# Kernel tuning notes

Hardware: AMD Instinct MI355X
Metric: run time of the kernel (lower is better)

Reference implementation:

```python
import jax, jax.numpy as jnp
import numpy as np

EPS = 1e-12
NEG_INF = -1e30

def _slog(x):
    return jnp.log(jnp.clip(x, EPS))

def setup_inputs() -> dict:
    M, Z = 24, 1024
    key = jax.random.key(0)
    ks = jax.random.split(key, 20)
    u = lambda k, sh, s=1.0: jax.random.uniform(k, sh, dtype=jnp.float32) * s
    demin = u(ks[0], (M, M), 0.2)
    demax = demin + u(ks[1], (M, M), 1.0)
    Kn = (jax.random.uniform(ks[2], (M, M)) > 0.5).astype(jnp.float32)
    # a couple of sectors with no substitution choices (rows stay all-ones in S)
    Kn = Kn.at[0].set(0.0).at[5].set(0.0)
    housing_mask = jnp.zeros((M,), dtype=bool).at[jnp.array([M - 2, M - 1])].set(True)
    genflux_mask = (jax.random.uniform(ks[3], (M,)) > 0.2)
    return {
        'h': jnp.zeros((M, Z), jnp.float32),
        'price': u(ks[4], (M, Z)),
        't_nij': u(ks[5], (M, Z, Z)),
        'demin': demin,
        'demax': demax,
        'delta': u(ks[6], (M, M), 0.2),
        'omega': u(ks[7], (M, M)),
        'sigma': u(ks[8], (M,), 0.5),
        'Kn': Kn,
        'attractor': u(ks[9], (M, Z)) + 0.1,
        'beta': u(ks[10], (M,), 0.5),
        'lamda': u(ks[11], (M,)),
        'A_ni': u(ks[12], (M, Z)) + 0.1,
        'exog_demand': u(ks[13], (M, Z)),
        'exog_prod': u(ks[14], (M, Z)),
        'X_0': u(ks[15], (M, Z)) + 0.1,
        'X_target': u(ks[16], (M, Z)),
        'housing_mask': housing_mask,
        'genflux_mask': genflux_mask,
    }

def reference(h, price, t_nij, demin, demax, delta, omega, sigma, Kn,
              attractor, beta, lamda, A_ni, exog_demand, exog_prod,
              X_0, X_target, housing_mask, genflux_mask):
    M, Z = price.shape
    ph = price + h                                            # [n,i] prices + shadow prices
    # LocationProbability: U_nij = lamda_n*ph[n,j] + t_nij; Pr = softmax_j for genflux non-housing, else eye
    U_nij = lamda[:, None, None] * ph[:, None, :] + t_nij     # [n,i,j]
    loc_logits = _slog(A_ni)[:, None, :] - beta[:, None, None] * U_nij
    Pr_soft = jax.nn.softmax(loc_logits, axis=-1)
    loc_mask = genflux_mask & (~housing_mask)                 # sectors with location choice
    eye = jnp.eye(Z, dtype=price.dtype)
    Pr = jnp.where(loc_mask[:, None, None], Pr_soft, eye[None, :, :])  # [n,i,j]
    # composite (expected) disutility per sector/zone
    U_ni = jnp.einsum('nij,nij->ni', Pr, U_nij)               # [n,i]
    # DemandFunction: a[m,n,i] = demin + (demax-demin)*exp(-delta*U_ni)
    a_mni = demin[:, :, None] + (demax - demin)[:, :, None] * jnp.exp(-delta[:, :, None] * U_ni[None])
    # SubstitutionProbability: masked softmax over substitutes n (axis=1), S=1 where no choice
    U_tilde = omega[:, :, None] * a_mni * U_ni[None]          # [m,n,i]
    cmask = (Kn > 0)[:, :, None]                              # [m,n,1]
    sub_logits = jnp.where(cmask, _slog(attractor)[None] - sigma[:, None, None] * U_tilde, NEG_INF)
    S_mni = jnp.where(cmask, jax.nn.softmax(sub_logits, axis=1), 1.0)
    # TotalDemand: D[n,i] = exog_demand + sum_m a*S*(X_0+exog_prod)
    X_total = X_0 + exog_prod
    D_ni = exog_demand + jnp.einsum('mni,mni,mi->ni', a_mni, S_mni, X_total)
    # induced production: X_pred[n,j] = sum_i D[n,i] * Pr[n,i,j]
    X_pred = jnp.einsum('ni,nij->nj', D_ni, Pr)
    return jnp.mean((X_pred - X_target) ** 2)
```

## Files before the change

kernel.cpp:

```cpp
#include <hip/hip_runtime.h>
#include <hip/hip_bf16.h>
#include <math.h>

#define MDIM 24
#define ZDIM 1024
#define NEG_INF_F -1e30f
#define EPS_F 1e-12f

enum {
  OFF_U    = 0,
  OFF_RMAX = 24576,
  OFF_SEXP = 49152,
  OFF_W    = 73728,
  OFF_XP   = 98304
};

__device__ __forceinline__ bool masks_are_bytes(const void* hm, const void* gm) {
  const unsigned int* hw = (const unsigned int*)hm;
  const unsigned int* gw = (const unsigned int*)gm;
  bool b = false;
  #pragma unroll
  for (int k = 0; k < 6; k++) {
    unsigned int a = hw[k], c = gw[k];
    if (a != 0u && a != 1u && a != 0x3F800000u) b = true;
    if (c != 0u && c != 1u && c != 0x3F800000u) b = true;
  }
  return b;
}
__device__ __forceinline__ bool loc_flag(const void* hm, const void* gm, int n) {
  bool bytes = masks_are_bytes(hm, gm);
  bool hv = bytes ? (((const unsigned char*)hm)[n] != 0)
                  : (((const unsigned int*)hm)[n] != 0u);
  bool gv = bytes ? (((const unsigned char*)gm)[n] != 0)
                  : (((const unsigned int*)gm)[n] != 0u);
  return gv && !hv;
}

__global__ __launch_bounds__(256) void k1_rows(
    const float* __restrict__ t, const float* __restrict__ price,
    const float* __restrict__ h, const float* __restrict__ A_ni,
    const float* __restrict__ beta, const float* __restrict__ lamda,
    const void* __restrict__ housing, const void* __restrict__ genflux,
    float* __restrict__ ws) {
  const int n  = blockIdx.x >> 6;
  const int i0 = (blockIdx.x & 63) * 16;
  const float bn = beta[n], ln = lamda[n];
  if (!loc_flag(housing, genflux, n)) {
    if (threadIdx.x < 16) {
      const int row = n * ZDIM + i0 + threadIdx.x;
      ws[OFF_U + row] = ln * (price[row] + h[row])
                        + t[(size_t)row * ZDIM + (i0 + threadIdx.x)];
    }
    return;
  }
  __shared__ float pc_s[ZDIM];
  __shared__ float cc_s[ZDIM];
  for (int j = threadIdx.x; j < ZDIM; j += 256) {
    const float pc = ln * (price[n * ZDIM + j] + h[n * ZDIM + j]);
    const float sa = logf(fmaxf(A_ni[n * ZDIM + j], EPS_F));
    pc_s[j] = pc;
    cc_s[j] = sa - bn * pc;
  }
  __syncthreads();
  const int wave = threadIdx.x >> 6, lane = threadIdx.x & 63;
  const float4* pc4 = (const float4*)pc_s;
  const float4* cc4 = (const float4*)cc_s;
  const int r0 = n * ZDIM + i0 + wave * 4;

  float4 tv[4][4];
  #pragma unroll
  for (int r = 0; r < 4; r++) {
    const float4* tp = (const float4*)(t + (size_t)(r0 + r) * ZDIM);
    tv[r][0] = tp[lane];
    tv[r][1] = tp[lane + 64];
    tv[r][2] = tp[lane + 128];
    tv[r][3] = tp[lane + 192];
  }

  #pragma unroll
  for (int r = 0; r < 4; r++) {
    float lg[16], uv[16];
    float mx = -INFINITY;
    #pragma unroll
    for (int k = 0; k < 4; k++) {
      const int f = lane + 64 * k;
      const float4 tt = tv[r][k];
      const float4 pv = pc4[f];
      const float4 cv = cc4[f];
      uv[4*k+0] = pv.x + tt.x;  lg[4*k+0] = cv.x - bn * tt.x;
      uv[4*k+1] = pv.y + tt.y;  lg[4*k+1] = cv.y - bn * tt.y;
      uv[4*k+2] = pv.z + tt.z;  lg[4*k+2] = cv.z - bn * tt.z;
      uv[4*k+3] = pv.w + tt.w;  lg[4*k+3] = cv.w - bn * tt.w;
      mx = fmaxf(mx, fmaxf(fmaxf(lg[4*k], lg[4*k+1]), fmaxf(lg[4*k+2], lg[4*k+3])));
    }
    #pragma unroll
    for (int off = 32; off >= 1; off >>= 1)
      mx = fmaxf(mx, __shfl_xor(mx, off));
    float se = 0.f, su = 0.f;
    #pragma unroll
    for (int k = 0; k < 16; k++) {
      const float e = __expf(lg[k] - mx);
      se += e;
      su = fmaf(e, uv[k], su);
    }
    #pragma unroll
    for (int off = 32; off >= 1; off >>= 1) {
      se += __shfl_xor(se, off);
      su += __shfl_xor(su, off);
    }
    if (lane == 0) {
      const int row = r0 + r;
      ws[OFF_U + row]    = su / se;
      ws[OFF_RMAX + row] = mx;
      ws[OFF_SEXP + row] = se;
    }
  }
}

__global__ __launch_bounds__(256) void k2_demand(
    const float* __restrict__ demin, const float* __restrict__ demax,
    const float* __restrict__ delta, const float* __restrict__ omega,
    const float* __restrict__ sigma, const float* __restrict__ Kn,
    const float* __restrict__ attractor, const float* __restrict__ exogd,
    const float* __restrict__ X0, const float* __restrict__ exogp,
    const void* __restrict__ housing, const void* __restrict__ genflux,
    float* __restrict__ ws) {
  const int wave = threadIdx.x >> 6;
  const int lane = threadIdx.x & 63;
  const int half = lane >> 5;
  const int n    = lane & 31;
  const int i    = blockIdx.x * 8 + wave * 2 + half;
  const bool nv  = (n < MDIM);
  float Uv = 0.f, asl = NEG_INF_F;
  if (nv) {
    Uv  = ws[OFF_U + n * ZDIM + i];
    asl = logf(fmaxf(attractor[n * ZDIM + i], EPS_F));
  }
  float acc = 0.f;
  for (int m = 0; m < MDIM; m++) {
    const float Xt  = X0[m * ZDIM + i] + exogp[m * ZDIM + i];
    const float sig = sigma[m];
    float dm = 0.f, dd = 0.f, dl = 0.f, om = 0.f, kn = 0.f;
    if (nv) {
      dm = demin[m * MDIM + n];
      dd = demax[m * MDIM + n] - dm;
      dl = delta[m * MDIM + n];
      om = omega[m * MDIM + n];
      kn = Kn[m * MDIM + n];
    }
    const float a = dm + dd * __expf(-dl * Uv);
    const bool valid = nv && (kn > 0.f);
    const float l = valid ? asl - sig * om * a * Uv : NEG_INF_F;
    float mx = l;
    #pragma unroll
    for (int off = 16; off >= 1; off >>= 1)
      mx = fmaxf(mx, __shfl_xor(mx, off));
    const float e = valid ? __expf(l - mx) : 0.f;
    float se = e;
    #pragma unroll
    for (int off = 16; off >= 1; off >>= 1)
      se += __shfl_xor(se, off);
    const float S = (valid && se > 0.f) ? e / se : 1.0f;
    if (nv) acc = fmaf(a * S, Xt, acc);
  }
  if (nv) {
    const float Dv = exogd[n * ZDIM + i] + acc;
    if (loc_flag(housing, genflux, n)) {
      ws[OFF_W  + n * ZDIM + i] = Dv / ws[OFF_SEXP + n * ZDIM + i];
      ws[OFF_XP + n * ZDIM + i] = 0.f;
    } else {
      ws[OFF_XP + n * ZDIM + i] = Dv;
    }
  }
}

__global__ __launch_bounds__(256) void k3_xpred(
    const float* __restrict__ t, const float* __restrict__ price,
    const float* __restrict__ h, const float* __restrict__ A_ni,
    const float* __restrict__ beta, const float* __restrict__ lamda,
    const void* __restrict__ housing, const void* __restrict__ genflux,
    float* __restrict__ ws) {
  const int n = blockIdx.x >> 6, ic = blockIdx.x & 63;
  if (!loc_flag(housing, genflux, n)) return;
  const int tj = threadIdx.x;
  const float bn = beta[n], ln = lamda[n];
  const float4 pr = ((const float4*)(price + n * ZDIM))[tj];
  const float4 hh = ((const float4*)(h     + n * ZDIM))[tj];
  const float4 aa = ((const float4*)(A_ni  + n * ZDIM))[tj];
  const float c0 = logf(fmaxf(aa.x, EPS_F)) - bn * (ln * (pr.x + hh.x));
  const float c1 = logf(fmaxf(aa.y, EPS_F)) - bn * (ln * (pr.y + hh.y));
  const float c2 = logf(fmaxf(aa.z, EPS_F)) - bn * (ln * (pr.z + hh.z));
  const float c3 = logf(fmaxf(aa.w, EPS_F)) - bn * (ln * (pr.w + hh.w));
  const float4* t4 = (const float4*)t;
  const int base = n * ZDIM + ic * 16;
  float4 tv[4];
  float  mx[4], w[4];
  #pragma unroll
  for (int r = 0; r < 4; r++) {
    tv[r] = t4[(size_t)(base + r) * (ZDIM / 4) + tj];
    mx[r] = ws[OFF_RMAX + base + r];
    w[r]  = ws[OFF_W + base + r];
  }
  float x0 = 0.f, x1 = 0.f, x2 = 0.f, x3 = 0.f;
  #pragma unroll
  for (int ii = 0; ii < 16; ii++) {
    const int s = ii & 3;
    const float4 cv = tv[s];
    const float  m  = mx[s], wt = w[s];
    if (ii < 12) {
      tv[s] = t4[(size_t)(base + ii + 4) * (ZDIM / 4) + tj];
      mx[s] = ws[OFF_RMAX + base + ii + 4];
      w[s]  = ws[OFF_W + base + ii + 4];
    }
    x0 = fmaf(wt, __expf(c0 - m - bn * cv.x), x0);
    x1 = fmaf(wt, __expf(c1 - m - bn * cv.y), x1);
    x2 = fmaf(wt, __expf(c2 - m - bn * cv.z), x2);
    x3 = fmaf(wt, __expf(c3 - m - bn * cv.w), x3);
  }
  float* xp = ws + OFF_XP + n * ZDIM + tj * 4;
  atomicAdd(xp + 0, x0);
  atomicAdd(xp + 1, x1);
  atomicAdd(xp + 2, x2);
  atomicAdd(xp + 3, x3);
}

__global__ __launch_bounds__(1024) void k4_loss(
    const float* __restrict__ Xtg, const float* __restrict__ ws,
    float* __restrict__ out) {
  float s = 0.f;
  for (int e = threadIdx.x; e < MDIM * ZDIM; e += 1024) {
    const float d = ws[OFF_XP + e] - Xtg[e];
    s = fmaf(d, d, s);
  }
  #pragma unroll
  for (int off = 32; off >= 1; off >>= 1) s += __shfl_xor(s, off);
  __shared__ float red[16];
  const int w = threadIdx.x >> 6, lane = threadIdx.x & 63;
  if (lane == 0) red[w] = s;
  __syncthreads();
  if (threadIdx.x == 0) {
    float tot = 0.f;
    #pragma unroll
    for (int k = 0; k < 16; k++) tot += red[k];
    *out = tot * (1.0f / (MDIM * ZDIM));
  }
}

extern "C" void kernel_launch(void* const* d_in, const int* in_sizes, int n_in,
                              void* d_out, int out_size, void* d_ws, size_t ws_size,
                              hipStream_t stream) {
  (void)in_sizes; (void)n_in; (void)out_size; (void)ws_size;
  const float* h       = (const float*)d_in[0];
  const float* price   = (const float*)d_in[1];
  const float* t       = (const float*)d_in[2];
  const float* demin   = (const float*)d_in[3];
  const float* demax   = (const float*)d_in[4];
  const float* delta   = (const float*)d_in[5];
  const float* omega   = (const float*)d_in[6];
  const float* sigma   = (const float*)d_in[7];
  const float* Kn      = (const float*)d_in[8];
  const float* attract = (const float*)d_in[9];
  const float* beta    = (const float*)d_in[10];
  const float* lamda   = (const float*)d_in[11];
  const float* A_ni    = (const float*)d_in[12];
  const float* exogd   = (const float*)d_in[13];
  const float* exogp   = (const float*)d_in[14];
  const float* X0      = (const float*)d_in[15];
  const float* Xtg     = (const float*)d_in[16];
  const void*  housing = d_in[17];
  const void*  genflux = d_in[18];
  float* ws  = (float*)d_ws;
  float* out = (float*)d_out;

  k1_rows<<<MDIM * 64, 256, 0, stream>>>(t, price, h, A_ni, beta, lamda,
                                         housing, genflux, ws);
  k2_demand<<<128, 256, 0, stream>>>(demin, demax, delta, omega, sigma, Kn,
                                     attract, exogd, X0, exogp,
                                     housing, genflux, ws);
  k3_xpred<<<MDIM * 64, 256, 0, stream>>>(t, price, h, A_ni, beta, lamda,
                                          housing, genflux, ws);
  k4_loss<<<1, 1024, 0, stream>>>(Xtg, ws, out);
}
```

Baseline: 248.8 us.

## Fuse demand, production and loss kernels into one with last-block reduction

```diff
diff --git a/kernel.cpp b/kernel.cpp
--- a/kernel.cpp
+++ b/kernel.cpp
@@ -6,13 +6,14 @@
 #define ZDIM 1024
 #define NEG_INF_F -1e30f
 #define EPS_F 1e-12f
+#define GRID_NB (MDIM * 64)
 
 enum {
   OFF_U    = 0,
   OFF_RMAX = 24576,
   OFF_SEXP = 49152,
-  OFF_W    = 73728,
-  OFF_XP   = 98304
+  OFF_XP   = 73728,
+  OFF_CNT  = 98304
 };
 
 __device__ __forceinline__ bool masks_are_bytes(const void* hm, const void* gm) {
@@ -42,6 +43,8 @@
     const float* __restrict__ beta, const float* __restrict__ lamda,
     const void* __restrict__ housing, const void* __restrict__ genflux,
     float* __restrict__ ws) {
+  if (blockIdx.x == 0 && threadIdx.x == 0)
+    ((int*)(ws + OFF_CNT))[0] = 0;
   const int n  = blockIdx.x >> 6;
   const int i0 = (blockIdx.x & 63) * 16;
   const float bn = beta[n], ln = lamda[n];
@@ -53,6 +56,8 @@
     }
     return;
   }
+  if (threadIdx.x < 16)
+    ws[OFF_XP + n * ZDIM + i0 + threadIdx.x] = 0.f;
   __shared__ float pc_s[ZDIM];
   __shared__ float cc_s[ZDIM];
   for (int j = threadIdx.x; j < ZDIM; j += 256) {
@@ -76,7 +81,6 @@
     tv[r][2] = tp[lane + 128];
     tv[r][3] = tp[lane + 192];
   }
-
   #pragma unroll
   for (int r = 0; r < 4; r++) {
     float lg[16], uv[16];
@@ -117,133 +121,132 @@
   }
 }
 
-__global__ __launch_bounds__(256) void k2_demand(
+__global__ __launch_bounds__(256) void k234(
+    const float* __restrict__ t, const float* __restrict__ price,
+    const float* __restrict__ h, const float* __restrict__ A_ni,
+    const float* __restrict__ beta, const float* __restrict__ lamda,
     const float* __restrict__ demin, const float* __restrict__ demax,
     const float* __restrict__ delta, const float* __restrict__ omega,
     const float* __restrict__ sigma, const float* __restrict__ Kn,
     const float* __restrict__ attractor, const float* __restrict__ exogd,
     const float* __restrict__ X0, const float* __restrict__ exogp,
-    const void* __restrict__ housing, const void* __restrict__ genflux,
-    float* __restrict__ ws) {
-  const int wave = threadIdx.x >> 6;
-  const int lane = threadIdx.x & 63;
+    const float* __restrict__ Xtg, const void* __restrict__ housing,
+    const void* __restrict__ genflux, float* __restrict__ ws,
+    float* __restrict__ out) {
+  const int n = blockIdx.x >> 6, ic = blockIdx.x & 63;
+  const int i0 = ic * 16;
+  const bool lf = loc_flag(housing, genflux, n);
+  __shared__ float w_s[16], mx_s[16];
+  __shared__ bool  is_last;
+  __shared__ float red[4];
+
+  const int wave = threadIdx.x >> 6, lane = threadIdx.x & 63;
   const int half = lane >> 5;
-  const int n    = lane & 31;
-  const int i    = blockIdx.x * 8 + wave * 2 + half;
-  const bool nv  = (n < MDIM);
-  float Uv = 0.f, asl = NEG_INF_F;
-  if (nv) {
-    Uv  = ws[OFF_U + n * ZDIM + i];
-    asl = logf(fmaxf(attractor[n * ZDIM + i], EPS_F));
-  }
-  float acc = 0.f;
-  for (int m = 0; m < MDIM; m++) {
-    const float Xt  = X0[m * ZDIM + i] + exogp[m * ZDIM + i];
-    const float sig = sigma[m];
-    float dm = 0.f, dd = 0.f, dl = 0.f, om = 0.f, kn = 0.f;
+  const int np   = lane & 31;
+  const bool nv  = (np < MDIM);
+  const int hw   = wave * 2 + half;
+  for (int zz = hw; zz < 16; zz += 8) {
+    const int i = i0 + zz;
+    float Uv = 0.f, asl = NEG_INF_F;
     if (nv) {
-      dm = demin[m * MDIM + n];
-      dd = demax[m * MDIM + n] - dm;
-      dl = delta[m * MDIM + n];
-      om = omega[m * MDIM + n];
-      kn = Kn[m * MDIM + n];
-    }
-    const float a = dm + dd * __expf(-dl * Uv);
-    const bool valid = nv && (kn > 0.f);
-    const float l = valid ? asl - sig * om * a * Uv : NEG_INF_F;
-    float mx = l;
-    #pragma unroll
-    for (int off = 16; off >= 1; off >>= 1)
-      mx = fmaxf(mx, __shfl_xor(mx, off));
-    const float e = valid ? __expf(l - mx) : 0.f;
-    float se = e;
-    #pragma unroll
-    for (int off = 16; off >= 1; off >>= 1)
-      se += __shfl_xor(se, off);
-    const float S = (valid && se > 0.f) ? e / se : 1.0f;
-    if (nv) acc = fmaf(a * S, Xt, acc);
-  }
-  if (nv) {
-    const float Dv = exogd[n * ZDIM + i] + acc;
-    if (loc_flag(housing, genflux, n)) {
-      ws[OFF_W  + n * ZDIM + i] = Dv / ws[OFF_SEXP + n * ZDIM + i];
-      ws[OFF_XP + n * ZDIM + i] = 0.f;
-    } else {
-      ws[OFF_XP + n * ZDIM + i] = Dv;
-    }
-  }
-}
-
-__global__ __launch_bounds__(256) void k3_xpred(
-    const float* __restrict__ t, const float* __restrict__ price,
-    const float* __restrict__ h, const float* __restrict__ A_ni,
-    const float* __restrict__ beta, const float* __restrict__ lamda,
-    const void* __restrict__ housing, const void* __restrict__ genflux,
-    float* __restrict__ ws) {
-  const int n = blockIdx.x >> 6, ic = blockIdx.x & 63;
-  if (!loc_flag(housing, genflux, n)) return;
-  const int tj = threadIdx.x;
-  const float bn = beta[n], ln = lamda[n];
-  const float4 pr = ((const float4*)(price + n * ZDIM))[tj];
-  const float4 hh = ((const float4*)(h     + n * ZDIM))[tj];
-  const float4 aa = ((const float4*)(A_ni  + n * ZDIM))[tj];
-  const float c0 = logf(fmaxf(aa.x, EPS_F)) - bn * (ln * (pr.x + hh.x));
-  const float c1 = logf(fmaxf(aa.y, EPS_F)) - bn * (ln * (pr.y + hh.y));
-  const float c2 = logf(fmaxf(aa.z, EPS_F)) - bn * (ln * (pr.z + hh.z));
-  const float c3 = logf(fmaxf(aa.w, EPS_F)) - bn * (ln * (pr.w + hh.w));
-  const float4* t4 = (const float4*)t;
-  const int base = n * ZDIM + ic * 16;
-  float4 tv[4];
-  float  mx[4], w[4];
-  #pragma unroll
-  for (int r = 0; r < 4; r++) {
-    tv[r] = t4[(size_t)(base + r) * (ZDIM / 4) + tj];
-    mx[r] = ws[OFF_RMAX + base + r];
-    w[r]  = ws[OFF_W + base + r];
-  }
-  float x0 = 0.f, x1 = 0.f, x2 = 0.f, x3 = 0.f;
-  #pragma unroll
-  for (int ii = 0; ii < 16; ii++) {
-    const int s = ii & 3;
-    const float4 cv = tv[s];
-    const float  m  = mx[s], wt = w[s];
-    if (ii < 12) {
-      tv[s] = t4[(size_t)(base + ii + 4) * (ZDIM / 4) + tj];
-      mx[s] = ws[OFF_RMAX + base + ii + 4];
-      w[s]  = ws[OFF_W + base + ii + 4];
-    }
-    x0 = fmaf(wt, __expf(c0 - m - bn * cv.x), x0);
-    x1 = fmaf(wt, __expf(c1 - m - bn * cv.y), x1);
-    x2 = fmaf(wt, __expf(c2 - m - bn * cv.z), x2);
-    x3 = fmaf(wt, __expf(c3 - m - bn * cv.w), x3);
-  }
-  float* xp = ws + OFF_XP + n * ZDIM + tj * 4;
-  atomicAdd(xp + 0, x0);
-  atomicAdd(xp + 1, x1);
-  atomicAdd(xp + 2, x2);
-  atomicAdd(xp + 3, x3);
-}
-
-__global__ __launch_bounds__(1024) void k4_loss(
-    const float* __restrict__ Xtg, const float* __restrict__ ws,
-    float* __restrict__ out) {
+      Uv  = ws[OFF_U + np * ZDIM + i];
+      asl = logf(fmaxf(attractor[np * ZDIM + i], EPS_F));
+    }
+    float acc = 0.f;
+    for (int m = 0; m < MDIM; m++) {
+      const float Xt  = X0[m * ZDIM + i] + exogp[m * ZDIM + i];
+      const float sig = sigma[m];
+      float dm = 0.f, dd = 0.f, dl = 0.f, om = 0.f, kn = 0.f;
+      if (nv) {
+        dm = demin[m * MDIM + np];
+        dd = demax[m * MDIM + np] - dm;
+        dl = delta[m * MDIM + np];
+        om = omega[m * MDIM + np];
+        kn = Kn[m * MDIM + np];
+      }
+      const float a = dm + dd * __expf(-dl * Uv);
+      const bool valid = nv && (kn > 0.f);
+      const float l = valid ? asl - sig * om * a * Uv : NEG_INF_F;
+      float mx = l;
+      #pragma unroll
+      for (int off = 16; off >= 1; off >>= 1)
+        mx = fmaxf(mx, __shfl_xor(mx, off));
+      const float e = valid ? __expf(l - mx) : 0.f;
+      float se = e;
+      #pragma unroll
+      for (int off = 16; off >= 1; off >>= 1)
+        se += __shfl_xor(se, off);
+      const float S = (valid && se > 0.f) ? e / se : 1.0f;
+      if (nv) acc = fmaf(a * S, Xt, acc);
+    }
+    if (np == n) {
+      const float Dv = exogd[n * ZDIM + i] + acc;
+      if (lf) {
+        w_s[zz]  = Dv / ws[OFF_SEXP + n * ZDIM + i];
+        mx_s[zz] = ws[OFF_RMAX + n * ZDIM + i];
+      } else {
+        ws[OFF_XP + n * ZDIM + i] = Dv;
+      }
+    }
+  }
+  __syncthreads();
+
+  if (lf) {
+    const int tj = threadIdx.x;
+    const float bn = beta[n], ln = lamda[n];
+    const float4 pr = ((const float4*)(price + n * ZDIM))[tj];
+    const float4 hh = ((const float4*)(h     + n * ZDIM))[tj];
+    const float4 aa = ((const float4*)(A_ni  + n * ZDIM))[tj];
+    const float c0 = logf(fmaxf(aa.x, EPS_F)) - bn * (ln * (pr.x + hh.x));
+    const float c1 = logf(fmaxf(aa.y, EPS_F)) - bn * (ln * (pr.y + hh.y));
+    const float c2 = logf(fmaxf(aa.z, EPS_F)) - bn * (ln * (pr.z + hh.z));
+    const float c3 = logf(fmaxf(aa.w, EPS_F)) - bn * (ln * (pr.w + hh.w));
+    const float4* t4 = (const float4*)t;
+    const int base = n * ZDIM + i0;
+    float4 tv[4];
+    #pragma unroll
+    for (int r = 0; r < 4; r++)
+      tv[r] = t4[(size_t)(base + r) * (ZDIM / 4) + tj];
+    float x0 = 0.f, x1 = 0.f, x2 = 0.f, x3 = 0.f;
+    #pragma unroll
+    for (int ii = 0; ii < 16; ii++) {
+      const int s = ii & 3;
+      const float4 cv = tv[s];
+      const float  m  = mx_s[ii], wt = w_s[ii];
+      if (ii < 12)
+        tv[s] = t4[(size_t)(base + ii + 4) * (ZDIM / 4) + tj];
+      x0 = fmaf(wt, __expf(c0 - m - bn * cv.x), x0);
+      x1 = fmaf(wt, __expf(c1 - m - bn * cv.y), x1);
+      x2 = fmaf(wt, __expf(c2 - m - bn * cv.z), x2);
+      x3 = fmaf(wt, __expf(c3 - m - bn * cv.w), x3);
+    }
+    float* xp = ws + OFF_XP + n * ZDIM + tj * 4;
+    atomicAdd(xp + 0, x0);
+    atomicAdd(xp + 1, x1);
+    atomicAdd(xp + 2, x2);
+    atomicAdd(xp + 3, x3);
+  }
+
+  __threadfence();
+  __syncthreads();
+  if (threadIdx.x == 0) {
+    const int old = atomicAdd((int*)(ws + OFF_CNT), 1);
+    is_last = (old == GRID_NB - 1);
+  }
+  __syncthreads();
+  if (!is_last) return;
+  __threadfence();
   float s = 0.f;
-  for (int e = threadIdx.x; e < MDIM * ZDIM; e += 1024) {
+  for (int e = threadIdx.x; e < MDIM * ZDIM; e += 256) {
     const float d = ws[OFF_XP + e] - Xtg[e];
     s = fmaf(d, d, s);
   }
   #pragma unroll
   for (int off = 32; off >= 1; off >>= 1) s += __shfl_xor(s, off);
-  __shared__ float red[16];
-  const int w = threadIdx.x >> 6, lane = threadIdx.x & 63;
-  if (lane == 0) red[w] = s;
-  __syncthreads();
-  if (threadIdx.x == 0) {
-    float tot = 0.f;
-    #pragma unroll
-    for (int k = 0; k < 16; k++) tot += red[k];
-    *out = tot * (1.0f / (MDIM * ZDIM));
-  }
+  if (lane == 0) red[wave] = s;
+  __syncthreads();
+  if (threadIdx.x == 0)
+    *out = (red[0] + red[1] + red[2] + red[3]) * (1.0f / (MDIM * ZDIM));
 }
 
 extern "C" void kernel_launch(void* const* d_in, const int* in_sizes, int n_in,
@@ -272,12 +275,10 @@
   float* ws  = (float*)d_ws;
   float* out = (float*)d_out;
 
-  k1_rows<<<MDIM * 64, 256, 0, stream>>>(t, price, h, A_ni, beta, lamda,
-                                         housing, genflux, ws);
-  k2_demand<<<128, 256, 0, stream>>>(demin, demax, delta, omega, sigma, Kn,
-                                     attract, exogd, X0, exogp,
-                                     housing, genflux, ws);
-  k3_xpred<<<MDIM * 64, 256, 0, stream>>>(t, price, h, A_ni, beta, lamda,
-                                          housing, genflux, ws);
-  k4_loss<<<1, 1024, 0, stream>>>(Xtg, ws, out);
-}
+  k1_rows<<<GRID_NB, 256, 0, stream>>>(t, price, h, A_ni, beta, lamda,
+                                       housing, genflux, ws);
+  k234<<<GRID_NB, 256, 0, stream>>>(t, price, h, A_ni, beta, lamda,
+                                    demin, demax, delta, omega, sigma, Kn,
+                                    attract, exogd, X0, exogp, Xtg,
+                                    housing, genflux, ws, out);
+}
```

Result: slower. 448.4 us (+80.2%).
